# Optimization experiments

Hardware: AMD Instinct MI355X
Metric: run time of the kernel (lower is better)

Reference implementation:

```python
import jax, jax.numpy as jnp
import numpy as np

Lx, Ly, D, P = 4, 5, 4, 2
DEPTH = 5
TAU = 0.1
N = Lx * Ly
B = 64


def setup_inputs() -> dict:
    key = jax.random.key(0)
    k1, k2, k3 = jax.random.split(key, 3)
    # PEPS site tensors: [Lx, Ly, phys, up, down, left, right]; boundary bonds sliced to dim 1 at use.
    peps = jax.random.normal(k1, (Lx, Ly, P, D, D, D, D), dtype=jnp.float32) * 0.5
    # Two-site Trotter gate: expm(-tau * h) for a random symmetric two-body term h (4x4).
    h = jax.random.normal(k2, (4, 4), dtype=jnp.float32)
    h = 0.5 * (h + h.T)
    w, v = jnp.linalg.eigh(h)
    gate = (v * jnp.exp(-TAU * w)) @ v.T  # [4,4]
    x = jax.random.randint(k3, (B, N), 0, 2, dtype=jnp.int32)
    return {"x": x, "peps": peps, "gate": gate}


def _slice_boundary(site, i, j):
    # site: [p, u, d, l, r]; open boundary -> bond dim 1 on lattice edges
    if i == 0:
        site = site[:, :1]
    if i == Lx - 1:
        site = site[:, :, :1]
    if j == 0:
        site = site[:, :, :, :1]
    if j == Ly - 1:
        site = site[..., :1]
    return site


def _peps_statevector(peps):
    # Exact contraction of the open-boundary PEPS to the full 2^N statevector.
    rows = []
    for i in range(Lx):
        T = jnp.ones((1, 1, 1, 1), dtype=peps.dtype)  # [Pphys, Uup, Ddown, l]
        for j in range(Ly):
            s = _slice_boundary(peps[i, j], i, j)
            T = jnp.einsum('PUDl,pudlr->PpUuDdr', T, s)
            Pn, p, U, u, Dn, d, r = T.shape
            T = T.reshape(Pn * p, U * u, Dn * d, r)
        rows.append(T[..., 0])  # [2^Ly, up_bonds, down_bonds]
    S = jnp.ones((1, 1), dtype=peps.dtype)  # [Pphys, down_bonds]
    for row in rows:
        S = jnp.einsum('PU,QUD->PQD', S, row)
        a, b, c = S.shape
        S = S.reshape(a * b, c)
    return S[:, 0]  # [2^N]


def _apply_gate(psi, g, a, b):
    # g: [2,2,2,2] = gate[o1,o2,i1,i2]; psi: (2,)*N
    out = jnp.tensordot(g, psi, axes=([2, 3], [a, b]))
    return jnp.moveaxis(out, (0, 1), (a, b))


def _bonds():
    horiz = [((i, j), (i, j + 1)) for i in range(Lx) for j in range(Ly - 1)]
    vert = [((i, j), (i + 1, j)) for i in range(Lx - 1) for j in range(Ly)]
    return horiz + vert


def reference(x, peps, gate):
    psi = _peps_statevector(peps).reshape((2,) * N)
    g = gate.reshape(2, 2, 2, 2)
    bonds = _bonds()
    for _ in range(DEPTH):
        for (i1, j1), (i2, j2) in bonds:
            psi = _apply_gate(psi, g, i1 * Ly + j1, i2 * Ly + j2)
    psi = psi.reshape(-1)
    pw = 2 ** jnp.arange(N - 1, -1, -1, dtype=jnp.int32)
    idx = (x * pw).sum(axis=1)
    return psi[idx]  # [B] amplitudes
```

## Files before the change

### kernel.cpp

```cpp
#include <hip/hip_runtime.h>


#define PAD(i) ((i) + (((i) >> 4) << 2))
#define PIDX(i,j,p,u,d,l,r) (((((((i)*5+(j))*2+(p))*4+(u))*4+(d))*4+(l))*4+(r))

typedef float v4f __attribute__((ext_vector_type(4)));

static constexpr int COL0  = 0;
static constexpr int COL1  = 4096;
static constexpr int COL2  = COL1 + 1048576;
static constexpr int COL3  = COL2 + 1048576;
static constexpr int COL4  = COL3 + 1048576;
static constexpr int M01TO = COL4 + 4096;
static constexpr int M34TO = M01TO + 65536;
static constexpr int T12TO = M34TO + 65536;
static constexpr int PSIO  = T12TO + 1048576;
static constexpr int CNTO  = PSIO + 1048576;

__device__ __forceinline__ float agl(const float* p) {
  return __hip_atomic_load(p, __ATOMIC_RELAXED, __HIP_MEMORY_SCOPE_AGENT);
}
__device__ __forceinline__ void cohload2(const float* p0, const float* p1,
                                         v4f& a, v4f& b) {
  asm volatile(
      "global_load_dwordx4 %0, %2, off sc0 sc1\n\t"
      "global_load_dwordx4 %1, %3, off sc0 sc1\n\t"
      "s_waitcnt vmcnt(0)"
      : "=&v"(a), "=&v"(b)
      : "v"(p0), "v"(p1)
      : "memory");
}
__device__ __forceinline__ void cohstore(float* p, v4f v) {
  asm volatile("global_store_dwordx4 %0, %1, off sc0 sc1"
               :
               : "v"(p), "v"(v)
               : "memory");
}
__device__ __forceinline__ void cohstore1(float* p, float v) {
  asm volatile("global_store_dword %0, %1, off sc0 sc1"
               :
               : "v"(p), "v"(v)
               : "memory");
}
__device__ __forceinline__ void vmdrain() {
  asm volatile("s_waitcnt vmcnt(0)" ::: "memory");
}

__device__ __forceinline__ void gridbar(int* cnts, int gen) {
  vmdrain();
  __syncthreads();
  if (threadIdx.x == 0) {
    int* gc = cnts + (blockIdx.x >> 4) * 64;
    int* root = cnts + 1024;
    int prev = __hip_atomic_fetch_add(gc, 1, __ATOMIC_RELAXED,
                                      __HIP_MEMORY_SCOPE_AGENT);
    if ((prev & 15) == 15)
      __hip_atomic_fetch_add(root, 1, __ATOMIC_RELAXED,
                             __HIP_MEMORY_SCOPE_AGENT);
    while (__hip_atomic_load(root, __ATOMIC_RELAXED,
                             __HIP_MEMORY_SCOPE_AGENT) < gen * 16) {
      __builtin_amdgcn_s_sleep(2);
    }
  }
  __syncthreads();
}

template <int NB, int HI, int LO>
__device__ __forceinline__ void gate2(float* x, const float* __restrict__ g) {
  constexpr int H = 1 << HI, L = 1 << LO, N = 1 << NB;
#pragma unroll
  for (int o = 0; o < N; ++o) {
    if (o & (H | L)) continue;
    float v0 = x[o], v1 = x[o + L], v2 = x[o + H], v3 = x[o + H + L];
    x[o]         = g[0]  * v0 + g[1]  * v1 + g[2]  * v2 + g[3]  * v3;
    x[o + L]     = g[4]  * v0 + g[5]  * v1 + g[6]  * v2 + g[7]  * v3;
    x[o + H]     = g[8]  * v0 + g[9]  * v1 + g[10] * v2 + g[11] * v3;
    x[o + H + L] = g[12] * v0 + g[13] * v1 + g[14] * v2 + g[15] * v3;
  }
}

template <int ST>
__device__ __forceinline__ void vxf(float* s, const float* __restrict__ g, int b) {
  float x[16];
#pragma unroll
  for (int m = 0; m < 16; ++m) x[m] = s[PAD(b + m * ST)];
  gate2<4, 3, 2>(x, g);
  gate2<4, 2, 1>(x, g);
  gate2<4, 1, 0>(x, g);
#pragma unroll
  for (int m = 0; m < 16; ++m) s[PAD(b + m * ST)] = x[m];
}

template <int B2, int B1, int B0>
__device__ __forceinline__ void bondpair(float* s, const float* __restrict__ g,
                                         int t) {
  constexpr int MASK = (1 << B2) | (1 << B1) | (1 << B0);
  int b = 0, rem = t;
#pragma unroll
  for (int p = 0; p < 12; ++p) {
    if (!((MASK >> p) & 1)) {
      b |= (rem & 1) << p;
      rem >>= 1;
    }
  }
  float x[8];
#pragma unroll
  for (int m = 0; m < 8; ++m) {
    int off = ((m >> 2) & 1) * (1 << B2) + ((m >> 1) & 1) * (1 << B1) +
              (m & 1) * (1 << B0);
    x[m] = s[PAD(b + off)];
  }
  gate2<3, 2, 1>(x, g);
  gate2<3, 1, 0>(x, g);
#pragma unroll
  for (int m = 0; m < 8; ++m) {
    int off = ((m >> 2) & 1) * (1 << B2) + ((m >> 1) & 1) * (1 << B1) +
              (m & 1) * (1 << B0);
    s[PAD(b + off)] = x[m];
  }
}

__global__ __launch_bounds__(512) void k_all(const float* __restrict__ peps,
                                             const int* __restrict__ x,
                                             const float* __restrict__ gate,
                                             float* __restrict__ ws,
                                             float* __restrict__ out,
                                             int* __restrict__ cnt) {
  __shared__ float sm[8224];
  const int t = threadIdx.x;
  const int b = blockIdx.x;
  const int r3 = t & 255, half = t >> 8;
  float* psi = ws + PSIO;
  int gen = 0;

  if (b < 192) {
    float* p01 = sm;
    float* p23 = sm + 4096;
    int col = 1 + (b >> 6);
    int pb = b & 63;
#pragma unroll
    for (int k = 0; k < 8; ++k) {
      int e = k * 512 + t;
      int r12 = e & 15, l12 = (e >> 4) & 15, d2 = (e >> 8) & 3, p = e >> 10;
      int l1 = l12 >> 2, l2 = l12 & 3, r1 = r12 >> 2, r2 = r12 & 3;
      float s01 = 0.f, s23 = 0.f;
#pragma unroll
      for (int d = 0; d < 4; ++d) {
        s01 += peps[PIDX(0, col, (p >> 1), 0, d, l1, r1)] *
               peps[PIDX(1, col, (p & 1), d, d2, l2, r2)];
        s23 += peps[PIDX(2, col, (p >> 1), d2, d, l1, r1)] *
               peps[PIDX(3, col, (p & 1), d, 0, l2, r2)];
      }
      p01[e] = s01;
      p23[e] = s23;
    }
    __syncthreads();
    const int coloffs[3] = {COL1, COL2, COL3};
    float* outc = ws + coloffs[col - 1];
#pragma unroll
    for (int pp = 0; pp < 2; ++pp) {
      int part = pb * 2 + pp;
#pragma unroll
      for (int k = 0; k < 4; ++k) {
        int eq = part * 8192 + (k * 512 + t) * 4;
        int r34b = eq & 15;
        int r12 = (eq >> 4) & 15, l34 = (eq >> 8) & 15, l12 = (eq >> 12) & 15;
        int p = eq >> 16;
        int pa = p >> 2, pbv = p & 3;
        v4f acc = {0.f, 0.f, 0.f, 0.f};
#pragma unroll
        for (int d2 = 0; d2 < 4; ++d2) {
          float a01 = p01[((((pa * 4 + d2) << 4) | l12) << 4) | r12];
          const float4 b4 =
              *(const float4*)&p23[((((pbv * 4 + d2) << 4) | l34) << 4) | r34b];
          acc.x += a01 * b4.x;
          acc.y += a01 * b4.y;
          acc.z += a01 * b4.z;
          acc.w += a01 * b4.w;
        }
        cohstore(&outc[eq], acc);
      }
    }
  } else if (b < 194) {
    float* p01 = sm;
    float* p23 = sm + 4096;
    int col = (b == 192) ? 0 : 4;
    const int lsh = (col == 0) ? 0 : 2;
    const int rsh = (col == 4) ? 0 : 2;
    const int ldim = 1 << lsh, rdim = 1 << rsh;
    const int LLB = 2 * lsh, RRB = 2 * rsh;
    const int LL = 1 << LLB, RR = 1 << RRB;
    int n12 = (LL * RR) << 4;
    for (int e = t; e < n12; e += 512) {
      int r12 = e & (RR - 1);
      int l12 = (e >> RRB) & (LL - 1);
      int d2 = (e >> (RRB + LLB)) & 3;
      int p = e >> (RRB + LLB + 2);
      int l1 = l12 >> lsh, l2 = l12 & (ldim - 1);
      int r1 = r12 >> rsh, r2 = r12 & (rdim - 1);
      float s01 = 0.f, s23 = 0.f;
      for (int d = 0; d < 4; ++d) {
        s01 += peps[PIDX(0, col, (p >> 1), 0, d, l1, r1)] *
               peps[PIDX(1, col, (p & 1), d, d2, l2, r2)];
        s23 += peps[PIDX(2, col, (p >> 1), d2, d, l1, r1)] *
               peps[PIDX(3, col, (p & 1), d, 0, l2, r2)];
      }
      p01[e] = s01;
      p23[e] = s23;
    }
    __syncthreads();
    const int LB = 2 * LLB, RB = 2 * RRB;
    int total = 16 << (LB + RB);
    float* outc = ws + ((col == 0) ? COL0 : COL4);
    for (int e = t; e < total; e += 512) {
      int r = e & ((1 << RB) - 1);
      int l = (e >> RB) & ((1 << LB) - 1);
      int p = e >> (RB + LB);
      int r34 = r & (RR - 1), r12 = r >> RRB;
      int l34 = l & (LL - 1), l12 = l >> LLB;
      int pa = p >> 2, pbv = p & 3;
      float sacc = 0.f;
      for (int d2 = 0; d2 < 4; ++d2) {
        sacc += p01[((((pa * 4 + d2) << LLB) | l12) << RRB) | r12] *
                p23[((((pbv * 4 + d2) << LLB) | l34) << RRB) | r34];
      }
      cohstore1(&outc[e], sacc);
    }
  }
  gridbar(cnt, ++gen);

  {
    float* c3buf = sm;
    float* c4buf = sm + 4112;
    const float* col3 = ws + COL3;
    const float* col4 = ws + COL4;
    const int L3 = b;
    if (t < 256) {
      float v3[16], v4[16];
#pragma unroll
      for (int k = 0; k < 16; ++k) {
        v4[k] = agl(&col4[k * 256 + t]);
        v3[k] = agl(&col3[k * 65536 + L3 * 256 + t]);
      }
#pragma unroll
      for (int k = 0; k < 16; ++k) {
        c4buf[k * 257 + t] = v4[k];
        c3buf[k * 257 + t] = v3[k];
      }
    } else {
      int c0 = b >> 4, c1 = b & 15, R2 = t - 256;
      const float* col0 = ws + COL0 + c0 * 256;
      const float* col1 = ws + COL1 + c1 * 65536 + R2;
      float acc = 0.f;
      float a_[16], c_[16], an[16], cn[16];
#pragma unroll
      for (int j = 0; j < 16; ++j) {
        a_[j] = agl(&col0[j]);
        c_[j] = agl(&col1[j * 256]);
      }
#pragma unroll
      for (int ch = 0; ch < 16; ++ch) {
        if (ch < 15) {
#pragma unroll
          for (int j = 0; j < 16; ++j) {
            an[j] = agl(&col0[(ch + 1) * 16 + j]);
            cn[j] = agl(&col1[((ch + 1) * 16 + j) * 256]);
          }
        }
#pragma unroll
        for (int j = 0; j < 16; ++j) acc += a_[j] * c_[j];
        if (ch < 15) {
#pragma unroll
          for (int j = 0; j < 16; ++j) { a_[j] = an[j]; c_[j] = cn[j]; }
        }
      }
      cohstore1(&(ws + M01TO)[(c0 * 16 + c1) * 256 + R2], acc);
    }
    __syncthreads();
    if (t < 256) {
      int c3 = t >> 4, c4 = t & 15;
      float acc = 0.f;
      for (int B = 0; B < 256; ++B)
        acc += c3buf[c3 * 257 + B] * c4buf[c4 * 257 + B];
      cohstore1(&(ws + M34TO)[L3 * 256 + t], acc);
    }
  }
  gridbar(cnt, ++gen);

  {
    float* A = sm;
    const float* m01 = ws + M01TO;
    const float* col2 = ws + COL2;
    float* t012p = ws + T12TO;
    int c2 = b & 15, tg = b >> 4;
    {
      float tmp[8];
#pragma unroll
      for (int k = 0; k < 2; ++k)
#pragma unroll
        for (int j = 0; j < 4; ++j)
          tmp[k * 4 + j] = agl(&m01[tg * 4096 + (k * 512 + t) * 4 + j]);
#pragma unroll
      for (int k = 0; k < 2; ++k)
#pragma unroll
        for (int j = 0; j < 4; ++j)
          A[(k * 512 + t) * 4 + j] = tmp[k * 4 + j];
    }
    __syncthreads();
    float acc[8] = {};
    const float* cbase = col2 + c2 * 65536 + r3;
    float cur[32], nxt[32];
#pragma unroll
    for (int j = 0; j < 32; ++j) cur[j] = agl(&cbase[j * 256]);
#pragma unroll
    for (int ch = 0; ch < 8; ++ch) {
      if (ch < 7) {
#pragma unroll
        for (int j = 0; j < 32; ++j)
          nxt[j] = agl(&cbase[((ch + 1) * 32 + j) * 256]);
      }
#pragma unroll
      for (int jj = 0; jj < 32; jj += 4) {
        int R2 = ch * 32 + jj;
#pragma unroll
        for (int i = 0; i < 8; ++i) {
          float4 a4 = *(const float4*)&A[(half * 8 + i) * 256 + R2];
          acc[i] += a4.x * cur[jj] + a4.y * cur[jj + 1] + a4.z * cur[jj + 2] +
                    a4.w * cur[jj + 3];
        }
      }
      if (ch < 7) {
#pragma unroll
        for (int j = 0; j < 32; ++j) cur[j] = nxt[j];
      }
    }
#pragma unroll
    for (int i = 0; i < 8; ++i)
      cohstore1(&t012p[c2 * 65536 + (tg * 16 + half * 8 + i) * 256 + r3],
                acc[i]);
  }
  gridbar(cnt, ++gen);

  {
    float* A = sm;
    float* S = sm + 4096;
    const float* t012p = ws + T12TO;
    const float* m34t = ws + M34TO;
    int tg = b;
    {
      float tmp[8];
#pragma unroll
      for (int i = 0; i < 8; ++i)
        tmp[i] = agl(&t012p[(half * 8 + i) * 65536 + tg * 256 + r3]);
#pragma unroll
      for (int i = 0; i < 8; ++i) A[(half * 8 + i) * 256 + r3] = tmp[i];
    }
    __syncthreads();
    float acc[8] = {};
    const float* mbase = m34t + r3;
    float cur[32], nxt[32];
#pragma unroll
    for (int j = 0; j < 32; ++j) cur[j] = agl(&mbase[j * 256]);
#pragma unroll
    for (int ch = 0; ch < 8; ++ch) {
      if (ch < 7) {
#pragma unroll
        for (int j = 0; j < 32; ++j)
          nxt[j] = agl(&mbase[((ch + 1) * 32 + j) * 256]);
      }
#pragma unroll
      for (int jj = 0; jj < 32; jj += 4) {
        int L3 = ch * 32 + jj;
#pragma unroll
        for (int i = 0; i < 8; ++i) {
          float4 a4 = *(const float4*)&A[(half * 8 + i) * 256 + L3];
          acc[i] += a4.x * cur[jj] + a4.y * cur[jj + 1] + a4.z * cur[jj + 2] +
                    a4.w * cur[jj + 3];
        }
      }
      if (ch < 7) {
#pragma unroll
        for (int j = 0; j < 32; ++j) cur[j] = nxt[j];
      }
    }
#pragma unroll
    for (int i = 0; i < 8; ++i) S[(half * 8 + i) * 257 + r3] = acc[i];
    __syncthreads();
    int c3 = r3 >> 4, c2 = r3 & 15;
    int base = c3 * 65536 + (tg >> 4) * 256 + (tg & 15) * 16 + c2;
#pragma unroll
    for (int vv = 0; vv < 8; ++vv) {
      int v = half * 8 + vv;
      cohstore1(&psi[base + v * 4096], S[c2 * 257 + c3 * 16 + v]);
    }
  }
  gridbar(cnt, ++gen);

  float g[16];
#pragma unroll
  for (int i = 0; i < 16; ++i) g[i] = gate[i];
  float* s = sm;

  for (int it = 0; it < 5; ++it) {
    {
      int f0 = t * 4, f1 = (512 + t) * 4;
      v4f a, c;
      cohload2(psi + b * 4096 + f0, psi + b * 4096 + f1, a, c);
      *(v4f*)(s + PAD(f0)) = a;
      *(v4f*)(s + PAD(f1)) = c;
    }
    __syncthreads();
    bondpair<8, 4, 0>(s, g, t);
    __syncthreads();
    bondpair<9, 5, 1>(s, g, t);
    __syncthreads();
    bondpair<10, 6, 2>(s, g, t);
    __syncthreads();
    bondpair<11, 7, 3>(s, g, t);
    __syncthreads();
    if (t < 256) vxf<256>(s, g, t);
    __syncthreads();
    if (t < 256) vxf<16>(s, g, ((t >> 4) << 8) | (t & 15));
    __syncthreads();
    {
      int f0 = t * 4, f1 = (512 + t) * 4;
      cohstore(psi + b * 4096 + f0, *(const v4f*)(s + PAD(f0)));
      cohstore(psi + b * 4096 + f1, *(const v4f*)(s + PAD(f1)));
    }
    gridbar(cnt, ++gen);

    {
      int f0 = t * 4, f1 = (512 + t) * 4;
      int a0 = (f0 >> 8) * 65536 + ((f0 >> 4) & 15) * 4096 + b * 16 + (f0 & 15);
      int a1 = (f1 >> 8) * 65536 + ((f1 >> 4) & 15) * 4096 + b * 16 + (f1 & 15);
      v4f a, c;
      cohload2(psi + a0, psi + a1, a, c);
      *(v4f*)(s + PAD(f0)) = a;
      *(v4f*)(s + PAD(f1)) = c;
    }
    __syncthreads();
    bondpair<0, 8, 4>(s, g, t);
    __syncthreads();
    bondpair<1, 9, 5>(s, g, t);
    __syncthreads();
    bondpair<2, 10, 6>(s, g, t);
    __syncthreads();
    bondpair<3, 11, 7>(s, g, t);
    __syncthreads();
    if (t < 256) vxf<1>(s, g, t * 16);
    __syncthreads();
    if (t < 256) vxf<256>(s, g, t);
    __syncthreads();
    if (t < 256) vxf<16>(s, g, ((t >> 4) << 8) | (t & 15));
    __syncthreads();
    if (it == 4) {
      if (t < 64) {
        int idx = 0;
#pragma unroll
        for (int q = 0; q < 20; ++q) {
          int i = q / 5, j = q % 5;
          int pos = (j == 0) ? (11 - i)
                   : (j == 1) ? (7 - i)
                   : (j == 2) ? (3 - i)
                   : (j == 3) ? (19 - i)
                              : (15 - i);
          idx |= x[t * 20 + q] << pos;
        }
        if (((idx >> 4) & 255) == b) {
          int local = ((idx >> 16) & 15) * 256 + ((idx >> 12) & 15) * 16 +
                      (idx & 15);
          out[t] = s[PAD(local)];
        }
      }
    } else {
      int f0 = t * 4, f1 = (512 + t) * 4;
      int a0 = (f0 >> 8) * 65536 + ((f0 >> 4) & 15) * 4096 + b * 16 + (f0 & 15);
      int a1 = (f1 >> 8) * 65536 + ((f1 >> 4) & 15) * 4096 + b * 16 + (f1 & 15);
      cohstore(psi + a0, *(const v4f*)(s + PAD(f0)));
      cohstore(psi + a1, *(const v4f*)(s + PAD(f1)));
      gridbar(cnt, ++gen);
    }
  }
}

extern "C" void kernel_launch(void* const* d_in, const int* in_sizes, int n_in,
                              void* d_out, int out_size, void* d_ws, size_t ws_size,
                              hipStream_t stream) {
  const int* x = (const int*)d_in[0];
  const float* peps = (const float*)d_in[1];
  const float* gate = (const float*)d_in[2];
  float* ws = (float*)d_ws;
  float* out = (float*)d_out;
  int* cnt = (int*)(ws + CNTO);

  hipMemsetAsync((void*)cnt, 0, 1088 * sizeof(int), stream);

  k_all<<<256, 512, 0, stream>>>(peps, x, gate, ws, out, cnt);
}
```

Baseline: 200.2 us.

## Rework contraction GEMM stages with register-tiled vector loads and fewer blocks

Replaces the scalar per-thread dot-product loops in the M01, T012 and psi-assembly stages with a shared register-tiled GEMM helper. Each thread computes a 4x4 output tile from dwordx4 coherent loads, double-buffered with explicit vmcnt waits. The M01 stage now runs on 16 blocks with col0 staged in LDS. The T012 and final stages use 128 blocks that each process twice the rows, trading parallelism for reuse and wider loads. The aim is to cut global load instruction count and latency stalls in these phases, at the cost of more LDS and idle blocks during those phases.

Measured after the change: 212.9 us. 6.3% more time.

```diff
diff --git a/kernel.cpp b/kernel.cpp
--- a/kernel.cpp
+++ b/kernel.cpp
@@ -20,6 +20,10 @@
 __device__ __forceinline__ float agl(const float* p) {
   return __hip_atomic_load(p, __ATOMIC_RELAXED, __HIP_MEMORY_SCOPE_AGENT);
 }
+__device__ __forceinline__ void cohload1(const float* p, v4f& a) {
+  asm volatile("global_load_dwordx4 %0, %1, off sc0 sc1"
+               : "=&v"(a) : "v"(p) : "memory");
+}
 __device__ __forceinline__ void cohload2(const float* p0, const float* p1,
                                          v4f& a, v4f& b) {
   asm volatile(
@@ -44,6 +48,14 @@
 }
 __device__ __forceinline__ void vmdrain() {
   asm volatile("s_waitcnt vmcnt(0)" ::: "memory");
+}
+__device__ __forceinline__ void vmw8() {
+  asm volatile("s_waitcnt vmcnt(8)" ::: "memory");
+  __builtin_amdgcn_sched_barrier(0);
+}
+__device__ __forceinline__ void vmw0() {
+  asm volatile("s_waitcnt vmcnt(0)" ::: "memory");
+  __builtin_amdgcn_sched_barrier(0);
 }
 
 __device__ __forceinline__ void gridbar(int* cnts, int gen) {
@@ -65,6 +77,63 @@
   __syncthreads();
 }
 
+__device__ __forceinline__ void coh_gemm(const float* Bb, const float* Ar,
+                                         v4f acc[4]) {
+  v4f pa0, pa1, pa2, pa3, pa4, pa5, pa6, pa7;
+  v4f pb0, pb1, pb2, pb3, pb4, pb5, pb6, pb7;
+#define ISSUE8(buf, base)                                                      \
+  cohload1(Bb + ((base) + 0) * 256, buf##0);                                   \
+  cohload1(Bb + ((base) + 1) * 256, buf##1);                                   \
+  cohload1(Bb + ((base) + 2) * 256, buf##2);                                   \
+  cohload1(Bb + ((base) + 3) * 256, buf##3);                                   \
+  cohload1(Bb + ((base) + 4) * 256, buf##4);                                   \
+  cohload1(Bb + ((base) + 5) * 256, buf##5);                                   \
+  cohload1(Bb + ((base) + 6) * 256, buf##6);                                   \
+  cohload1(Bb + ((base) + 7) * 256, buf##7)
+#define FMA8(buf, base)                                                        \
+  {                                                                            \
+    _Pragma("unroll") for (int r = 0; r < 4; ++r) {                            \
+      acc[r] += buf##0 * Ar[r * 256 + (base) + 0];                             \
+      acc[r] += buf##1 * Ar[r * 256 + (base) + 1];                             \
+      acc[r] += buf##2 * Ar[r * 256 + (base) + 2];                             \
+      acc[r] += buf##3 * Ar[r * 256 + (base) + 3];                             \
+      acc[r] += buf##4 * Ar[r * 256 + (base) + 4];                             \
+      acc[r] += buf##5 * Ar[r * 256 + (base) + 5];                             \
+      acc[r] += buf##6 * Ar[r * 256 + (base) + 6];                             \
+      acc[r] += buf##7 * Ar[r * 256 + (base) + 7];                             \
+    }                                                                          \
+  }
+  ISSUE8(pa, 0);
+#pragma unroll
+  for (int cp = 0; cp < 16; ++cp) {
+    ISSUE8(pb, cp * 16 + 8);
+    vmw8();
+    FMA8(pa, cp * 16);
+    if (cp < 15) {
+      ISSUE8(pa, cp * 16 + 16);
+      vmw8();
+    } else {
+      vmw0();
+    }
+    FMA8(pb, cp * 16 + 8);
+  }
+#undef ISSUE8
+#undef FMA8
+}
+
+__device__ __forceinline__ void stage8k(const float* gsrc, float* lds, int t) {
+  v4f v0, v1, v2, v3;
+  cohload1(gsrc + (0 * 512 + t) * 4, v0);
+  cohload1(gsrc + (1 * 512 + t) * 4, v1);
+  cohload1(gsrc + (2 * 512 + t) * 4, v2);
+  cohload1(gsrc + (3 * 512 + t) * 4, v3);
+  vmw0();
+  *(v4f*)&lds[(0 * 512 + t) * 4] = v0;
+  *(v4f*)&lds[(1 * 512 + t) * 4] = v1;
+  *(v4f*)&lds[(2 * 512 + t) * 4] = v2;
+  *(v4f*)&lds[(3 * 512 + t) * 4] = v3;
+}
+
 template <int NB, int HI, int LO>
 __device__ __forceinline__ void gate2(float* x, const float* __restrict__ g) {
   constexpr int H = 1 << HI, L = 1 << LO, N = 1 << NB;
@@ -126,10 +195,10 @@
                                              float* __restrict__ ws,
                                              float* __restrict__ out,
                                              int* __restrict__ cnt) {
-  __shared__ float sm[8224];
+  __shared__ float sm[12320];
   const int t = threadIdx.x;
   const int b = blockIdx.x;
-  const int r3 = t & 255, half = t >> 8;
+  const int cg = t & 63;
   float* psi = ws + PSIO;
   int gen = 0;
 
@@ -232,8 +301,10 @@
   {
     float* c3buf = sm;
     float* c4buf = sm + 4112;
+    float* col0l = sm + 8224;
     const float* col3 = ws + COL3;
     const float* col4 = ws + COL4;
+    const float* col0g = ws + COL0;
     const int L3 = b;
     if (t < 256) {
       float v3[16], v4[16];
@@ -247,34 +318,10 @@
         c4buf[k * 257 + t] = v4[k];
         c3buf[k * 257 + t] = v3[k];
       }
-    } else {
-      int c0 = b >> 4, c1 = b & 15, R2 = t - 256;
-      const float* col0 = ws + COL0 + c0 * 256;
-      const float* col1 = ws + COL1 + c1 * 65536 + R2;
-      float acc = 0.f;
-      float a_[16], c_[16], an[16], cn[16];
-#pragma unroll
-      for (int j = 0; j < 16; ++j) {
-        a_[j] = agl(&col0[j]);
-        c_[j] = agl(&col1[j * 256]);
-      }
-#pragma unroll
-      for (int ch = 0; ch < 16; ++ch) {
-        if (ch < 15) {
-#pragma unroll
-          for (int j = 0; j < 16; ++j) {
-            an[j] = agl(&col0[(ch + 1) * 16 + j]);
-            cn[j] = agl(&col1[((ch + 1) * 16 + j) * 256]);
-          }
-        }
-#pragma unroll
-        for (int j = 0; j < 16; ++j) acc += a_[j] * c_[j];
-        if (ch < 15) {
-#pragma unroll
-          for (int j = 0; j < 16; ++j) { a_[j] = an[j]; c_[j] = cn[j]; }
-        }
-      }
-      cohstore1(&(ws + M01TO)[(c0 * 16 + c1) * 256 + R2], acc);
+    } else if (b < 16) {
+      int tt = t - 256;
+#pragma unroll
+      for (int k = 0; k < 16; ++k) col0l[k * 256 + tt] = agl(&col0g[k * 256 + tt]);
     }
     __syncthreads();
     if (t < 256) {
@@ -283,116 +330,78 @@
       for (int B = 0; B < 256; ++B)
         acc += c3buf[c3 * 257 + B] * c4buf[c4 * 257 + B];
       cohstore1(&(ws + M34TO)[L3 * 256 + t], acc);
+    } else if (b < 16) {
+      int rg = (t >> 6) & 3;
+      v4f acc[4] = {};
+      coh_gemm(ws + COL1 + b * 65536 + cg * 4, &col0l[rg * 4 * 256], acc);
+      float* m01p = ws + M01TO;
+#pragma unroll
+      for (int r = 0; r < 4; ++r)
+        cohstore(&m01p[((rg * 4 + r) * 16 + b) * 256 + cg * 4], acc[r]);
     }
   }
   gridbar(cnt, ++gen);
 
-  {
+  if (b < 128) {
     float* A = sm;
-    const float* m01 = ws + M01TO;
-    const float* col2 = ws + COL2;
+    int c2 = b & 15, hb = b >> 4;
+    stage8k(ws + M01TO + hb * 8192, A, t);
+    __syncthreads();
+    int rg = t >> 6;
+    v4f acc[4] = {};
+    coh_gemm(ws + COL2 + c2 * 65536 + cg * 4, &A[rg * 4 * 256], acc);
     float* t012p = ws + T12TO;
-    int c2 = b & 15, tg = b >> 4;
+#pragma unroll
+    for (int r = 0; r < 4; ++r)
+      cohstore(&t012p[c2 * 65536 + (hb * 32 + rg * 4 + r) * 256 + cg * 4],
+               acc[r]);
+  }
+  gridbar(cnt, ++gen);
+
+  if (b < 128) {
+    float* A = sm;
+    float* S = sm;
     {
-      float tmp[8];
-#pragma unroll
-      for (int k = 0; k < 2; ++k)
-#pragma unroll
-        for (int j = 0; j < 4; ++j)
-          tmp[k * 4 + j] = agl(&m01[tg * 4096 + (k * 512 + t) * 4 + j]);
-#pragma unroll
-      for (int k = 0; k < 2; ++k)
-#pragma unroll
-        for (int j = 0; j < 4; ++j)
-          A[(k * 512 + t) * 4 + j] = tmp[k * 4 + j];
-    }
-    __syncthreads();
-    float acc[8] = {};
-    const float* cbase = col2 + c2 * 65536 + r3;
-    float cur[32], nxt[32];
-#pragma unroll
-    for (int j = 0; j < 32; ++j) cur[j] = agl(&cbase[j * 256]);
-#pragma unroll
-    for (int ch = 0; ch < 8; ++ch) {
-      if (ch < 7) {
-#pragma unroll
-        for (int j = 0; j < 32; ++j)
-          nxt[j] = agl(&cbase[((ch + 1) * 32 + j) * 256]);
-      }
-#pragma unroll
-      for (int jj = 0; jj < 32; jj += 4) {
-        int R2 = ch * 32 + jj;
-#pragma unroll
-        for (int i = 0; i < 8; ++i) {
-          float4 a4 = *(const float4*)&A[(half * 8 + i) * 256 + R2];
-          acc[i] += a4.x * cur[jj] + a4.y * cur[jj + 1] + a4.z * cur[jj + 2] +
-                    a4.w * cur[jj + 3];
-        }
-      }
-      if (ch < 7) {
-#pragma unroll
-        for (int j = 0; j < 32; ++j) cur[j] = nxt[j];
-      }
-    }
-#pragma unroll
-    for (int i = 0; i < 8; ++i)
-      cohstore1(&t012p[c2 * 65536 + (tg * 16 + half * 8 + i) * 256 + r3],
-                acc[i]);
-  }
-  gridbar(cnt, ++gen);
-
-  {
-    float* A = sm;
-    float* S = sm + 4096;
-    const float* t012p = ws + T12TO;
-    const float* m34t = ws + M34TO;
-    int tg = b;
-    {
-      float tmp[8];
-#pragma unroll
-      for (int i = 0; i < 8; ++i)
-        tmp[i] = agl(&t012p[(half * 8 + i) * 65536 + tg * 256 + r3]);
-#pragma unroll
-      for (int i = 0; i < 8; ++i) A[(half * 8 + i) * 256 + r3] = tmp[i];
-    }
-    __syncthreads();
-    float acc[8] = {};
-    const float* mbase = m34t + r3;
-    float cur[32], nxt[32];
-#pragma unroll
-    for (int j = 0; j < 32; ++j) cur[j] = agl(&mbase[j * 256]);
-#pragma unroll
-    for (int ch = 0; ch < 8; ++ch) {
-      if (ch < 7) {
-#pragma unroll
-        for (int j = 0; j < 32; ++j)
-          nxt[j] = agl(&mbase[((ch + 1) * 32 + j) * 256]);
-      }
-#pragma unroll
-      for (int jj = 0; jj < 32; jj += 4) {
-        int L3 = ch * 32 + jj;
-#pragma unroll
-        for (int i = 0; i < 8; ++i) {
-          float4 a4 = *(const float4*)&A[(half * 8 + i) * 256 + L3];
-          acc[i] += a4.x * cur[jj] + a4.y * cur[jj + 1] + a4.z * cur[jj + 2] +
-                    a4.w * cur[jj + 3];
-        }
-      }
-      if (ch < 7) {
-#pragma unroll
-        for (int j = 0; j < 32; ++j) cur[j] = nxt[j];
-      }
-    }
-#pragma unroll
-    for (int i = 0; i < 8; ++i) S[(half * 8 + i) * 257 + r3] = acc[i];
-    __syncthreads();
-    int c3 = r3 >> 4, c2 = r3 & 15;
-    int base = c3 * 65536 + (tg >> 4) * 256 + (tg & 15) * 16 + c2;
-#pragma unroll
-    for (int vv = 0; vv < 8; ++vv) {
-      int v = half * 8 + vv;
-      cohstore1(&psi[base + v * 4096], S[c2 * 257 + c3 * 16 + v]);
-    }
+      v4f v0, v1, v2, v3;
+      const float* t012p = ws + T12TO;
+      int f0 = (0 * 512 + t) * 4, f1 = (1 * 512 + t) * 4;
+      int f2 = (2 * 512 + t) * 4, f3 = (3 * 512 + t) * 4;
+      cohload1(t012p + (((f0 >> 8) & 15) * 65536 + (2 * b + (f0 >> 12)) * 256 +
+                        (f0 & 255)), v0);
+      cohload1(t012p + (((f1 >> 8) & 15) * 65536 + (2 * b + (f1 >> 12)) * 256 +
+                        (f1 & 255)), v1);
+      cohload1(t012p + (((f2 >> 8) & 15) * 65536 + (2 * b + (f2 >> 12)) * 256 +
+                        (f2 & 255)), v2);
+      cohload1(t012p + (((f3 >> 8) & 15) * 65536 + (2 * b + (f3 >> 12)) * 256 +
+                        (f3 & 255)), v3);
+      vmw0();
+      *(v4f*)&A[f0] = v0;
+      *(v4f*)&A[f1] = v1;
+      *(v4f*)&A[f2] = v2;
+      *(v4f*)&A[f3] = v3;
+    }
+    __syncthreads();
+    int rg = t >> 6;
+    v4f acc[4] = {};
+    coh_gemm(ws + M34TO + cg * 4, &A[rg * 4 * 256], acc);
+    __syncthreads();
+#pragma unroll
+    for (int r = 0; r < 4; ++r) {
+      int ri = rg * 4 + r;
+      int sb = (ri >> 4) * 4112 + (ri & 15) * 257 + cg * 4;
+      S[sb + 0] = acc[r].x;
+      S[sb + 1] = acc[r].y;
+      S[sb + 2] = acc[r].z;
+      S[sb + 3] = acc[r].w;
+    }
+    __syncthreads();
+    int tid = t & 255, tgl = t >> 8;
+    int c3 = tid >> 4, c2v = tid & 15;
+    int tg = 2 * b + tgl;
+    int base = c3 * 65536 + (tg >> 4) * 256 + (tg & 15) * 16 + c2v;
+#pragma unroll
+    for (int v = 0; v < 16; ++v)
+      cohstore1(&psi[base + v * 4096], S[tgl * 4112 + c2v * 257 + c3 * 16 + v]);
   }
   gridbar(cnt, ++gen);
 
```
